# Performance work log

Measured on AMD Instinct MI355X. Metric: run time of the kernel, lower is better.

The kernel has to match this reference:

```python
import jax, jax.numpy as jnp
import numpy as np

THRESHOLD = 1.5
MIN_AREA = 3
B, H, W = 8, 1024, 1024


def _label_components(mask):
    """8-connectivity connected-component labeling by min-index propagation.
    mask: [B,H,W] bool. Returns int32 labels [B,H,W]; each component is labeled
    by the minimum global flat index of its pixels; background pixels = B*H*W.
    Labels are globally unique across the batch (matches sort_labels' per-batch
    unique relabeling up to a label permutation).
    """
    N = B * H * W
    SENT = jnp.int32(N)
    flat = jnp.arange(N, dtype=jnp.int32).reshape(B, H, W)
    lab0 = jnp.where(mask, flat, SENT)

    def neighbor_min(lab):
        p = jnp.pad(lab, ((0, 0), (1, 1), (1, 1)), constant_values=N)
        m = lab
        for dr in (-1, 0, 1):
            for dc in (-1, 0, 1):
                if dr == 0 and dc == 0:
                    continue
                m = jnp.minimum(m, p[:, 1 + dr:1 + dr + H, 1 + dc:1 + dc + W])
        return jnp.where(mask, m, SENT)

    def cond(state):
        return state[1]

    def body(state):
        lab, _ = state
        new = neighbor_min(lab)
        return new, jnp.any(new != lab)

    lab, _ = jax.lax.while_loop(cond, body, (lab0, jnp.array(True)))
    return lab


def setup_inputs() -> dict:
    key = jax.random.key(0)
    x = jax.random.normal(key, (B, H, W // 1), dtype=jnp.float32)
    return {"input_tensor": x.reshape(B, 1, H, W)}


def reference(input_tensor):
    """Dense encoding of the original ragged output: for every pixel belonging
    to a cluster with area > MIN_AREA, emit the cluster's max value and the
    (row, col) of the first (lowest flat index) occurrence of that max;
    background / small-cluster pixels get (0, -1, -1). Since THRESHOLD > 0,
    max over masked_fill(0) in the original equals max over cluster pixels.
    """
    x = input_tensor[:, 0]                  # [B,H,W]
    N = B * H * W
    nseg = N + 1                            # last segment = background
    mask = (x >= THRESHOLD)
    ids = _label_components(mask).reshape(-1)          # [N] int32 in [0, N]
    vals = x.reshape(-1)
    fg = mask.reshape(-1)

    area = jax.ops.segment_sum(fg.astype(jnp.float32), ids, num_segments=nseg)
    cmax = jax.ops.segment_max(vals, ids, num_segments=nseg)

    within = jnp.tile(jnp.arange(H * W, dtype=jnp.int32), B)  # flat idx in image
    is_max = (vals == cmax[ids]) & fg
    cand = jnp.where(is_max, within, jnp.int32(H * W))
    amin = jax.ops.segment_min(cand, ids, num_segments=nseg)  # first argmax

    valid = fg & (area[ids] > MIN_AREA)
    out_max = jnp.where(valid, cmax[ids], jnp.float32(0.0)).reshape(B, H, W)
    aidx = amin[ids]
    row = jnp.where(valid, aidx // W, jnp.int32(-1)).reshape(B, H, W)
    col = jnp.where(valid, aidx % W, jnp.int32(-1)).reshape(B, H, W)
    return out_max, row, col
```

## Files before the change

### kernel.cpp

```cpp
#include <hip/hip_runtime.h>
#include <stdint.h>

#define THRESH 1.5f
constexpr int NPIX = 8 * 1024 * 1024;
constexpr int HW   = 1024 * 1024;
constexpr int WW   = 1024;
constexpr int NWORD = NPIX / 32;
constexpr int WPR   = WW / 32;

constexpr int BLK     = 256;
constexpr int GRD_PX4 = NPIX / (BLK * 4);
constexpr int GRD_W   = NWORD / BLK;

constexpr int SPB        = 640;
constexpr int BASE_SLOTS = GRD_W * SPB;
constexpr int OVF_SLOTS  = 16384;
constexpr int CAP        = BASE_SLOTS + OVF_SLOTS;

constexpr int WLSTRIDE = 1024;

__device__ __forceinline__ int find_root(const int* __restrict__ P, int x) {
    int p = P[x];
    while (p != x && p < NPIX) { x = p; p = P[x]; }
    return x;
}

__device__ __forceinline__ void merge(int* P, int a, int b) {
    int ra = find_root(P, a);
    int rb = find_root(P, b);
    while (ra != rb) {
        if (ra < rb) { int t = ra; ra = rb; rb = t; }
        int old = atomicCAS(&P[ra], ra, rb);
        if (old == ra) break;
        ra = find_root(P, old);
        rb = find_root(P, rb);
    }
}

__global__ void mask_init_k(const float* __restrict__ x, int* __restrict__ parent,
                            unsigned* __restrict__ mask, uint2* __restrict__ wl,
                            int* __restrict__ wl_cnt, int* __restrict__ ovf,
                            float* __restrict__ o) {
    __shared__ unsigned s_nib[BLK];
    __shared__ int s_rank;
    int t  = threadIdx.x;
    int gt = blockIdx.x * BLK + t;
    int i4 = gt * 4;
    float4 v = *(const float4*)(x + i4);
    unsigned nib = (unsigned)(v.x >= THRESH) | ((unsigned)(v.y >= THRESH) << 1) |
                   ((unsigned)(v.z >= THRESH) << 2) | ((unsigned)(v.w >= THRESH) << 3);
    *(float4*)(o + i4)            = make_float4(0.f, 0.f, 0.f, 0.f);
    *(float4*)(o + NPIX + i4)     = make_float4(-1.f, -1.f, -1.f, -1.f);
    *(float4*)(o + 2 * NPIX + i4) = make_float4(-1.f, -1.f, -1.f, -1.f);
    if (nib)
        *(int4*)(parent + i4) = make_int4(i4, i4 + 1, i4 + 2, i4 + 3);
    if (t == 0) s_rank = 0;
    s_nib[t] = nib;
    __syncthreads();
    if ((t & 7) == 0) {
        unsigned w = 0;
        #pragma unroll
        for (int k = 0; k < 8; k++) w |= s_nib[t + k] << (4 * k);
        mask[gt >> 3] = w;
    }
    int nfg = __popc(nib);
    if (nfg) {
        int r = atomicAdd(&s_rank, nfg);
        uint2* dst = wl + (size_t)blockIdx.x * WLSTRIDE;
        if (nib & 1u) dst[r++] = make_uint2((unsigned)i4,     __float_as_uint(v.x));
        if (nib & 2u) dst[r++] = make_uint2((unsigned)i4 + 1, __float_as_uint(v.y));
        if (nib & 4u) dst[r++] = make_uint2((unsigned)i4 + 2, __float_as_uint(v.z));
        if (nib & 8u) dst[r++] = make_uint2((unsigned)i4 + 3, __float_as_uint(v.w));
    }
    __syncthreads();
    if (t == 0) wl_cnt[blockIdx.x] = s_rank;
    if (gt == 0) *ovf = 0;
}

__global__ void union_k(const unsigned* __restrict__ mask, int* __restrict__ parent) {
    int w = blockIdx.x * BLK + threadIdx.x;
    unsigned cur = mask[w];
    if (!cur) return;
    int r  = (w >> 5) & (WW - 1);
    int cw = w & (WPR - 1);
    unsigned prev = (cw > 0) ? mask[w - 1] : 0u;
    unsigned above = 0u, abovePrev = 0u, aboveNext = 0u;
    if (r > 0) {
        above     = mask[w - WPR];
        abovePrev = (cw > 0)       ? mask[w - WPR - 1] : 0u;
        aboveNext = (cw < WPR - 1) ? mask[w - WPR + 1] : 0u;
    }
    int base = w << 5;
    unsigned mW  = cur & ((cur   << 1) | (prev      >> 31));
    unsigned mN  = cur & above;
    unsigned mNW = cur & ((above << 1) | (abovePrev >> 31));
    unsigned mNE = cur & ((above >> 1) | ((aboveNext & 1u) << 31));
    while (mW)  { int b = __ffs(mW)  - 1; mW  &= mW  - 1; merge(parent, base + b, base + b - 1); }
    while (mN)  { int b = __ffs(mN)  - 1; mN  &= mN  - 1; merge(parent, base + b, base + b - WW); }
    while (mNW) { int b = __ffs(mNW) - 1; mNW &= mNW - 1; merge(parent, base + b, base + b - WW - 1); }
    while (mNE) { int b = __ffs(mNE) - 1; mNE &= mNE - 1; merge(parent, base + b, base + b - WW + 1); }
}

__global__ void claim_k(const unsigned* __restrict__ mask, int* __restrict__ parent,
                        int* __restrict__ cnt, unsigned long long* __restrict__ best,
                        int* __restrict__ ovf) {
    __shared__ int s_cnt;
    if (threadIdx.x == 0) s_cnt = 0;
    __syncthreads();
    int w = blockIdx.x * BLK + threadIdx.x;
    unsigned cur = mask[w];
    int base = w << 5;
    while (cur) {
        int b = __ffs(cur) - 1; cur &= cur - 1;
        int p = base + b;
        int root = find_root(parent, p);
        if (root == p) {
            int rank = atomicAdd(&s_cnt, 1);
            int slot;
            if (rank < SPB) slot = blockIdx.x * SPB + rank;
            else { int o = atomicAdd(ovf, 1); slot = BASE_SLOTS + (o < OVF_SLOTS ? o : OVF_SLOTS - 1); }
            cnt[slot] = 0; best[slot] = 0ull;
            parent[p] = NPIX + slot;
        } else {
            parent[p] = root;
        }
    }
}

__device__ __forceinline__ int compact_id(const int* __restrict__ P, int p) {
    int e = P[p];
    if (e < NPIX) e = P[e];
    return e - NPIX;
}

__global__ void stats_k(uint2* __restrict__ wl, const int* __restrict__ wl_cnt,
                        const int* __restrict__ parent, int* __restrict__ cnt,
                        unsigned long long* __restrict__ best) {
    int region = blockIdx.x;
    int c = wl_cnt[region];
    uint2* src = wl + (size_t)region * WLSTRIDE;
    for (int j = threadIdx.x; j < c; j += 64) {
        uint2 e = src[j];
        int p = (int)e.x;
        int cid = compact_id(parent, p);
        if (cid < 0 || cid >= CAP) { src[j].y = 0xFFFFFFFFu; continue; }
        src[j].y = (unsigned)cid;
        atomicAdd(&cnt[cid], 1);
        unsigned within = (unsigned)(p & (HW - 1));
        unsigned long long pk =
            ((unsigned long long)e.y << 32) | (unsigned long long)(~within);
        atomicMax(&best[cid], pk);
    }
}

__global__ void scatter_k(const uint2* __restrict__ wl, const int* __restrict__ wl_cnt,
                          const int* __restrict__ cnt,
                          const unsigned long long* __restrict__ best,
                          float* __restrict__ o) {
    int region = blockIdx.x;
    int c = wl_cnt[region];
    const uint2* src = wl + (size_t)region * WLSTRIDE;
    for (int j = threadIdx.x; j < c; j += 64) {
        uint2 e = src[j];
        unsigned cid = e.y;
        if (cid >= (unsigned)CAP) continue;
        if (cnt[cid] > 3) {
            unsigned long long pk = best[cid];
            unsigned idx = ~((unsigned)pk);
            int p = (int)e.x;
            o[p]            = __uint_as_float((unsigned)(pk >> 32));
            o[p + NPIX]     = (float)(idx >> 10);
            o[p + 2 * NPIX] = (float)(idx & (WW - 1));
        }
    }
}

extern "C" void kernel_launch(void* const* d_in, const int* in_sizes, int n_in,
                              void* d_out, int out_size, void* d_ws, size_t ws_size,
                              hipStream_t stream) {
    const float* x = (const float*)d_in[0];
    float* o = (float*)d_out;

    char* base = (char*)d_ws;
    int* parent = (int*)base;
    size_t off = (size_t)NPIX * 4;
    unsigned long long* best = (unsigned long long*)(base + off);  off += (size_t)CAP * 8;
    int* cnt       = (int*)(base + off);                           off += (size_t)CAP * 4;
    unsigned* mask = (unsigned*)(base + off);                      off += (size_t)NWORD * 4;
    int* wl_cnt    = (int*)(base + off);                           off += (size_t)GRD_PX4 * 4;
    uint2* wl      = (uint2*)(base + off);                         off += (size_t)GRD_PX4 * WLSTRIDE * 8;
    int* ovf       = (int*)(base + off);

    mask_init_k<<<GRD_PX4, BLK, 0, stream>>>(x, parent, mask, wl, wl_cnt, ovf, o);
    union_k    <<<GRD_W,   BLK, 0, stream>>>(mask, parent);
    claim_k    <<<GRD_W,   BLK, 0, stream>>>(mask, parent, cnt, best, ovf);
    stats_k    <<<GRD_PX4, 64,  0, stream>>>(wl, wl_cnt, parent, cnt, best);
    scatter_k  <<<GRD_PX4, 64,  0, stream>>>(wl, wl_cnt, cnt, best, o);
}
```

Baseline: 206.9 us.

## Fuse root claiming into stats kernel and pre-zero slot tables in init

Removes the separate claim kernel, which walked the whole bitmask and ran find_root on every foreground pixel. Root-to-slot assignment now happens lazily inside the stats kernel through an atomicCAS on the root's parent entry, drawing from per-region slot ranges. The cnt/best tables are zeroed up front in mask_init with vectorized stores. Non-root pixels no longer get path-compressed, so stats-time finds may walk longer chains, and CAS races can let a block burn slots it never uses.

```diff
diff --git a/kernel.cpp b/kernel.cpp
--- a/kernel.cpp
+++ b/kernel.cpp
@@ -12,35 +12,36 @@
 constexpr int GRD_PX4 = NPIX / (BLK * 4);
 constexpr int GRD_W   = NWORD / BLK;
 
-constexpr int SPB        = 640;
-constexpr int BASE_SLOTS = GRD_W * SPB;
+constexpr int SPB        = 192;
+constexpr int BASE_SLOTS = GRD_PX4 * SPB;
 constexpr int OVF_SLOTS  = 16384;
 constexpr int CAP        = BASE_SLOTS + OVF_SLOTS;
+constexpr int ZB16       = CAP * 12 / 16;
 
 constexpr int WLSTRIDE = 1024;
 
-__device__ __forceinline__ int find_root(const int* __restrict__ P, int x) {
+__device__ __forceinline__ int find_node(const int* __restrict__ P, int x) {
     int p = P[x];
     while (p != x && p < NPIX) { x = p; p = P[x]; }
     return x;
 }
 
 __device__ __forceinline__ void merge(int* P, int a, int b) {
-    int ra = find_root(P, a);
-    int rb = find_root(P, b);
+    int ra = find_node(P, a);
+    int rb = find_node(P, b);
     while (ra != rb) {
         if (ra < rb) { int t = ra; ra = rb; rb = t; }
         int old = atomicCAS(&P[ra], ra, rb);
         if (old == ra) break;
-        ra = find_root(P, old);
-        rb = find_root(P, rb);
+        ra = find_node(P, old);
+        rb = find_node(P, rb);
     }
 }
 
 __global__ void mask_init_k(const float* __restrict__ x, int* __restrict__ parent,
                             unsigned* __restrict__ mask, uint2* __restrict__ wl,
                             int* __restrict__ wl_cnt, int* __restrict__ ovf,
-                            float* __restrict__ o) {
+                            uint4* __restrict__ zbase, float* __restrict__ o) {
     __shared__ unsigned s_nib[BLK];
     __shared__ int s_rank;
     int t  = threadIdx.x;
@@ -52,6 +53,7 @@
     *(float4*)(o + i4)            = make_float4(0.f, 0.f, 0.f, 0.f);
     *(float4*)(o + NPIX + i4)     = make_float4(-1.f, -1.f, -1.f, -1.f);
     *(float4*)(o + 2 * NPIX + i4) = make_float4(-1.f, -1.f, -1.f, -1.f);
+    if (gt < ZB16) zbase[gt] = make_uint4(0u, 0u, 0u, 0u);
     if (nib)
         *(int4*)(parent + i4) = make_int4(i4, i4 + 1, i4 + 2, i4 + 3);
     if (t == 0) s_rank = 0;
@@ -101,48 +103,32 @@
     while (mNE) { int b = __ffs(mNE) - 1; mNE &= mNE - 1; merge(parent, base + b, base + b - WW + 1); }
 }
 
-__global__ void claim_k(const unsigned* __restrict__ mask, int* __restrict__ parent,
-                        int* __restrict__ cnt, unsigned long long* __restrict__ best,
+__global__ void stats_k(uint2* __restrict__ wl, const int* __restrict__ wl_cnt,
+                        int* __restrict__ parent, int* __restrict__ cnt,
+                        unsigned long long* __restrict__ best,
                         int* __restrict__ ovf) {
-    __shared__ int s_cnt;
-    if (threadIdx.x == 0) s_cnt = 0;
+    __shared__ int s_rank;
+    if (threadIdx.x == 0) s_rank = 0;
     __syncthreads();
-    int w = blockIdx.x * BLK + threadIdx.x;
-    unsigned cur = mask[w];
-    int base = w << 5;
-    while (cur) {
-        int b = __ffs(cur) - 1; cur &= cur - 1;
-        int p = base + b;
-        int root = find_root(parent, p);
-        if (root == p) {
-            int rank = atomicAdd(&s_cnt, 1);
-            int slot;
-            if (rank < SPB) slot = blockIdx.x * SPB + rank;
-            else { int o = atomicAdd(ovf, 1); slot = BASE_SLOTS + (o < OVF_SLOTS ? o : OVF_SLOTS - 1); }
-            cnt[slot] = 0; best[slot] = 0ull;
-            parent[p] = NPIX + slot;
-        } else {
-            parent[p] = root;
-        }
-    }
-}
-
-__device__ __forceinline__ int compact_id(const int* __restrict__ P, int p) {
-    int e = P[p];
-    if (e < NPIX) e = P[e];
-    return e - NPIX;
-}
-
-__global__ void stats_k(uint2* __restrict__ wl, const int* __restrict__ wl_cnt,
-                        const int* __restrict__ parent, int* __restrict__ cnt,
-                        unsigned long long* __restrict__ best) {
     int region = blockIdx.x;
     int c = wl_cnt[region];
     uint2* src = wl + (size_t)region * WLSTRIDE;
     for (int j = threadIdx.x; j < c; j += 64) {
         uint2 e = src[j];
         int p = (int)e.x;
-        int cid = compact_id(parent, p);
+        int r = find_node(parent, p);
+        int pe = parent[r];
+        int cid;
+        if (pe >= NPIX) {
+            cid = pe - NPIX;
+        } else {
+            int rank = atomicAdd(&s_rank, 1);
+            int slot;
+            if (rank < SPB) slot = region * SPB + rank;
+            else { int ov = atomicAdd(ovf, 1); slot = BASE_SLOTS + (ov < OVF_SLOTS ? ov : OVF_SLOTS - 1); }
+            int old = atomicCAS(&parent[r], r, NPIX + slot);
+            cid = (old == r) ? slot : (old - NPIX);
+        }
         if (cid < 0 || cid >= CAP) { src[j].y = 0xFFFFFFFFu; continue; }
         src[j].y = (unsigned)cid;
         atomicAdd(&cnt[cid], 1);
@@ -184,6 +170,7 @@
     char* base = (char*)d_ws;
     int* parent = (int*)base;
     size_t off = (size_t)NPIX * 4;
+    uint4* zbase = (uint4*)(base + off);
     unsigned long long* best = (unsigned long long*)(base + off);  off += (size_t)CAP * 8;
     int* cnt       = (int*)(base + off);                           off += (size_t)CAP * 4;
     unsigned* mask = (unsigned*)(base + off);                      off += (size_t)NWORD * 4;
@@ -191,9 +178,8 @@
     uint2* wl      = (uint2*)(base + off);                         off += (size_t)GRD_PX4 * WLSTRIDE * 8;
     int* ovf       = (int*)(base + off);
 
-    mask_init_k<<<GRD_PX4, BLK, 0, stream>>>(x, parent, mask, wl, wl_cnt, ovf, o);
+    mask_init_k<<<GRD_PX4, BLK, 0, stream>>>(x, parent, mask, wl, wl_cnt, ovf, zbase, o);
     union_k    <<<GRD_W,   BLK, 0, stream>>>(mask, parent);
-    claim_k    <<<GRD_W,   BLK, 0, stream>>>(mask, parent, cnt, best, ovf);
-    stats_k    <<<GRD_PX4, 64,  0, stream>>>(wl, wl_cnt, parent, cnt, best);
+    stats_k    <<<GRD_PX4, 64,  0, stream>>>(wl, wl_cnt, parent, cnt, best, ovf);
     scatter_k  <<<GRD_PX4, 64,  0, stream>>>(wl, wl_cnt, cnt, best, o);
 }
```

Result: slower. 218.5 us (+5.6%).
